# Kernel tuning notes

Measured on AMD Instinct MI355X. Metric: run time of the kernel, lower is better.

Reference implementation:

```python
import jax, jax.numpy as jnp
import numpy as np

D_MODEL = 1024
NUM_HEADS = 16
THETA = 10000.0
B, S = 4, 2048


def setup_inputs() -> dict:
    key = jax.random.key(0)
    ks = jax.random.split(key, 5)
    scale = 1.0 / np.sqrt(D_MODEL)  # keep logits in a sane range
    return {
        "q_proj_weight": jax.random.normal(ks[0], (D_MODEL, D_MODEL), jnp.float32) * scale,
        "k_proj_weight": jax.random.normal(ks[1], (D_MODEL, D_MODEL), jnp.float32) * scale,
        "v_proj_weight": jax.random.normal(ks[2], (D_MODEL, D_MODEL), jnp.float32) * scale,
        "o_proj_weight": jax.random.normal(ks[3], (D_MODEL, D_MODEL), jnp.float32) * scale,
        "in_features": jax.random.normal(ks[4], (B, S, D_MODEL), jnp.float32),
        "token_positions": jnp.arange(S, dtype=jnp.int32),
    }


def _rope(x, cos, sin):
    # interleaved-pair RoPE: pairs are (x[..., 2i], x[..., 2i+1])
    xe = x[..., 0::2]
    xo = x[..., 1::2]
    re = xe * cos - xo * sin
    ro = xe * sin + xo * cos
    return jnp.stack([re, ro], axis=-1).reshape(x.shape)


def reference(q_proj_weight, k_proj_weight, v_proj_weight, o_proj_weight,
              in_features, token_positions):
    Bv, Sv, _ = in_features.shape
    dk = D_MODEL // NUM_HEADS
    half = dk // 2

    q = in_features @ q_proj_weight.T
    k = in_features @ k_proj_weight.T
    v = in_features @ v_proj_weight.T
    # (B, S, D) -> (B, H, S, dk)
    q = q.reshape(Bv, Sv, NUM_HEADS, dk).transpose(0, 2, 1, 3)
    k = k.reshape(Bv, Sv, NUM_HEADS, dk).transpose(0, 2, 1, 3)
    v = v.reshape(Bv, Sv, NUM_HEADS, dk).transpose(0, 2, 1, 3)

    inv_freq = 1.0 / (THETA ** (jnp.arange(half, dtype=jnp.float32) / half))
    freqs = token_positions.astype(jnp.float32)[:, None] * inv_freq[None, :]  # (S, half)
    cos, sin = jnp.cos(freqs), jnp.sin(freqs)  # broadcast over (B, H, S, half)
    q = _rope(q, cos, sin)
    k = _rope(k, cos, sin)

    scores = jnp.einsum('bhqd,bhkd->bhqk', q, k) / np.sqrt(dk).astype(np.float32)
    causal = jnp.tril(jnp.ones((Sv, Sv), dtype=bool))
    scores = jnp.where(causal, scores, -jnp.inf)
    weights = jax.nn.softmax(scores, axis=-1)
    out = jnp.einsum('bhqk,bhkd->bhqd', weights, v)
    out = out.transpose(0, 2, 1, 3).reshape(Bv, Sv, D_MODEL)
    return out @ o_proj_weight.T
```

## Files before the change

### kernel.cpp

```cpp
#include <hip/hip_runtime.h>
#include <stdint.h>
#include <math.h>

#define NH 16
#define DK 64
#define S_LEN 2048
#define BB 4
#define DM 1024
#define M_TOT (BB*S_LEN)
#define KVT 64
#define KPAD 72
#define QB 128

#define BM 256
#define BN 128
#define BK 64
#define NTK (DM/BK)
#define LDS_A_BUF (BM*BK)
#define LDS_B_BUF (BN*BK)

typedef __attribute__((ext_vector_type(8))) short short8;
typedef __attribute__((ext_vector_type(4))) float floatx4;

typedef const __attribute__((address_space(1))) void gas_t;
typedef __attribute__((address_space(3))) void las_t;

__device__ __forceinline__ void glds16(const void* g, void* l){
  __builtin_amdgcn_global_load_lds((gas_t*)g, (las_t*)l, 16, 0, 0);
}

#define VMCNT3() asm volatile("s_waitcnt vmcnt(3)" ::: "memory")
#define VMCNT6() asm volatile("s_waitcnt vmcnt(6)" ::: "memory")
#define VMCNT0() asm volatile("s_waitcnt vmcnt(0)" ::: "memory")
#define LGKM0()  do{ asm volatile("s_waitcnt lgkmcnt(0)" ::: "memory"); __builtin_amdgcn_sched_barrier(0); }while(0)
#define BARRIER() asm volatile("s_barrier" ::: "memory")
#define SCHEDB() __builtin_amdgcn_sched_barrier(0)

__device__ __forceinline__ unsigned short f2bf(float f){
  unsigned int u = __float_as_uint(f);
  u += 0x7fffu + ((u >> 16) & 1u);
  return (unsigned short)(u >> 16);
}
__device__ __forceinline__ unsigned int pk_bf_trunc(float a, float b){
  return __builtin_amdgcn_perm(__float_as_uint(b), __float_as_uint(a), 0x07060302u);
}
__device__ __forceinline__ float fast_exp2(float x){
  return __builtin_amdgcn_exp2f(x);
}

__global__ void cast_kernel(const float* __restrict__ in, unsigned short* __restrict__ out, int n){
  int i = (blockIdx.x * blockDim.x + threadIdx.x) * 4;
  if (i < n){
    float4 v = *(const float4*)(in + i);
    ushort4 u;
    u.x = f2bf(v.x); u.y = f2bf(v.y); u.z = f2bf(v.z); u.w = f2bf(v.w);
    *(ushort4*)(out + i) = u;
  }
}
__global__ void cast4_kernel(const float* __restrict__ a, const float* __restrict__ b,
                             const float* __restrict__ c, const float* __restrict__ d,
                             unsigned short* __restrict__ oa, unsigned short* __restrict__ ob,
                             unsigned short* __restrict__ oc, unsigned short* __restrict__ od){
  int z = blockIdx.y;
  const float* s = (z==0)?a:(z==1)?b:(z==2)?c:d;
  unsigned short* o = (z==0)?oa:(z==1)?ob:(z==2)?oc:od;
  int i = (blockIdx.x * blockDim.x + threadIdx.x) * 4;
  float4 v = *(const float4*)(s + i);
  ushort4 u;
  u.x = f2bf(v.x); u.y = f2bf(v.y); u.z = f2bf(v.z); u.w = f2bf(v.w);
  *(ushort4*)(o + i) = u;
}

__device__ __forceinline__ void stage_part(const unsigned short* __restrict__ A,
                                           const unsigned short* __restrict__ Bm,
                                           int m0, int n0, int k0,
                                           unsigned short* As, unsigned short* Bs,
                                           int tid, int part)
{
  if (part == 0){
    #pragma unroll
    for (int j = 0; j < 2; j++){
      int c = j*512 + tid;
      int r = c >> 3;
      int sl = (c & 7) ^ (r & 7);
      glds16(&A[(size_t)(m0 + r)*DM + k0 + sl*8], (char*)As + (size_t)c*16);
    }
    int c = tid;
    int r = c >> 3;
    int sl = (c & 7) ^ (r & 7);
    glds16(&Bm[(size_t)(n0 + r)*DM + k0 + sl*8], (char*)Bs + (size_t)c*16);
  } else {
    #pragma unroll
    for (int j = 2; j < 4; j++){
      int c = j*512 + tid;
      int r = c >> 3;
      int sl = (c & 7) ^ (r & 7);
      glds16(&A[(size_t)(m0 + r)*DM + k0 + sl*8], (char*)As + (size_t)c*16);
    }
    int c = 512 + tid;
    int r = c >> 3;
    int sl = (c & 7) ^ (r & 7);
    glds16(&Bm[(size_t)(n0 + r)*DM + k0 + sl*8], (char*)Bs + (size_t)c*16);
  }
}

__device__ __forceinline__ void gemm_core(const unsigned short* __restrict__ A,
                                          const unsigned short* __restrict__ Bm,
                                          int m0, int n0, unsigned short* Ls,
                                          int tid, floatx4 (&acc)[4][4])
{
  unsigned short* AsB = Ls;
  unsigned short* BsB = Ls + 3*LDS_A_BUF;
  int wave = tid >> 6, lane = tid & 63;
  int l15 = lane & 15, quad = lane >> 4;
  int wm = (wave >> 1) * 64, wn = (wave & 1) * 64;
  int s0 = quad ^ (l15 & 7);

  short8 a01[2][2], a23[2][2], b[2][4][2];

  stage_part(A, Bm, m0, n0, 0,  AsB,             BsB,             tid, 0);
  stage_part(A, Bm, m0, n0, 0,  AsB,             BsB,             tid, 1);
  stage_part(A, Bm, m0, n0, BK, AsB + LDS_A_BUF, BsB + LDS_B_BUF, tid, 0);
  stage_part(A, Bm, m0, n0, BK, AsB + LDS_A_BUF, BsB + LDS_B_BUF, tid, 1);
  VMCNT6();
  BARRIER();
  #pragma unroll
  for (int mi = 0; mi < 2; mi++){
    const unsigned short* pr = AsB + (wm + mi*16 + l15)*BK;
    a01[mi][0] = *(const short8*)(pr + s0*8);
    a01[mi][1] = *(const short8*)(pr + (s0^4)*8);
  }
  #pragma unroll
  for (int ni = 0; ni < 4; ni++){
    const unsigned short* pr = BsB + (wn + ni*16 + l15)*BK;
    b[0][ni][0] = *(const short8*)(pr + s0*8);
    b[0][ni][1] = *(const short8*)(pr + (s0^4)*8);
  }

  #pragma unroll
  for (int t = 0; t < NTK; ++t){
    const int par = t & 1, nxt = par ^ 1;
    const unsigned short* Ab  = AsB + (t % 3)*LDS_A_BUF;
    const unsigned short* Abn = AsB + ((t+1) % 3)*LDS_A_BUF;
    const unsigned short* Bbn = BsB + ((t+1) % 3)*LDS_B_BUF;
    unsigned short* Ast = AsB + ((t+2) % 3)*LDS_A_BUF;
    unsigned short* Bst = BsB + ((t+2) % 3)*LDS_B_BUF;
    const int kst = (t + 2) * BK;

    LGKM0();
    #pragma unroll
    for (int mi = 0; mi < 2; mi++){
      const unsigned short* pr = Ab + (wm + (2+mi)*16 + l15)*BK;
      a23[mi][0] = *(const short8*)(pr + s0*8);
      a23[mi][1] = *(const short8*)(pr + (s0^4)*8);
    }
    if (t + 2 < NTK) stage_part(A, Bm, m0, n0, kst, Ast, Bst, tid, 0);
    SCHEDB();
    __builtin_amdgcn_s_setprio(1);
    #pragma unroll
    for (int mi = 0; mi < 2; mi++)
      #pragma unroll
      for (int ni = 0; ni < 4; ni++){
        acc[mi][ni] = __builtin_amdgcn_mfma_f32_16x16x32_bf16(a01[mi][0], b[par][ni][0], acc[mi][ni], 0, 0, 0);
        acc[mi][ni] = __builtin_amdgcn_mfma_f32_16x16x32_bf16(a01[mi][1], b[par][ni][1], acc[mi][ni], 0, 0, 0);
      }
    __builtin_amdgcn_s_setprio(0);
    if (t + 2 < NTK)      { VMCNT3(); }
    else if (t + 1 < NTK) { VMCNT0(); }
    BARRIER();

    LGKM0();
    if (t + 1 < NTK){
      #pragma unroll
      for (int mi = 0; mi < 2; mi++){
        const unsigned short* pr = Abn + (wm + mi*16 + l15)*BK;
        a01[mi][0] = *(const short8*)(pr + s0*8);
        a01[mi][1] = *(const short8*)(pr + (s0^4)*8);
      }
      #pragma unroll
      for (int ni = 0; ni < 4; ni++){
        const unsigned short* pr = Bbn + (wn + ni*16 + l15)*BK;
        b[nxt][ni][0] = *(const short8*)(pr + s0*8);
        b[nxt][ni][1] = *(const short8*)(pr + (s0^4)*8);
      }
    }
    if (t + 2 < NTK) stage_part(A, Bm, m0, n0, kst, Ast, Bst, tid, 1);
    SCHEDB();
    __builtin_amdgcn_s_setprio(1);
    #pragma unroll
    for (int mi = 0; mi < 2; mi++)
      #pragma unroll
      for (int ni = 0; ni < 4; ni++){
        acc[2+mi][ni] = __builtin_amdgcn_mfma_f32_16x16x32_bf16(a23[mi][0], b[par][ni][0], acc[2+mi][ni], 0, 0, 0);
        acc[2+mi][ni] = __builtin_amdgcn_mfma_f32_16x16x32_bf16(a23[mi][1], b[par][ni][1], acc[2+mi][ni], 0, 0, 0);
      }
    __builtin_amdgcn_s_setprio(0);
    if (t + 1 < NTK) BARRIER();
  }
}

__global__ __launch_bounds__(512, 2) void gemm_qkv(
    const unsigned short* __restrict__ Xb,
    const unsigned short* __restrict__ Wq,
    const unsigned short* __restrict__ Wk,
    const unsigned short* __restrict__ Wv,
    const int* __restrict__ pos,
    unsigned short* __restrict__ Qo,
    unsigned short* __restrict__ Ko,
    unsigned short* __restrict__ VTo)
{
  __shared__ __align__(16) unsigned short Ls[3*LDS_A_BUF + 3*LDS_B_BUF];
  int m0 = blockIdx.x * BM;
  int n0 = blockIdx.y * BN;
  int z  = blockIdx.z;
  const unsigned short* Bmat = (z == 0) ? Wq : ((z == 1) ? Wk : Wv);
  unsigned short* Out = (z == 0) ? Qo : ((z == 1) ? Ko : VTo);

  int tid = threadIdx.x;
  floatx4 acc[4][4] = {};
  gemm_core(Xb, Bmat, m0, n0, Ls, tid, acc);

  int wave = tid >> 6, lane = tid & 63;
  int l15 = lane & 15, quad = lane >> 4;
  int wm = (wave >> 1) * 64, wn = (wave & 1) * 64;

  if (z == 2){
    #pragma unroll
    for (int mi = 0; mi < 4; mi++){
      int row0 = m0 + wm + mi * 16 + quad * 4;
      int bb2 = row0 >> 11, sQ = row0 & (S_LEN - 1);
      #pragma unroll
      for (int ni = 0; ni < 4; ni++){
        int col = n0 + wn + ni * 16 + l15;
        int h = col >> 6, d = col & 63;
        ushort4 u;
        u.x = f2bf(acc[mi][ni][0]); u.y = f2bf(acc[mi][ni][1]);
        u.z = f2bf(acc[mi][ni][2]); u.w = f2bf(acc[mi][ni][3]);
        *(ushort4*)&Out[(((size_t)bb2 * NH + h) * DK + d) * S_LEN + sQ] = u;
      }
    }
  } else {
    const float SC = (z == 0) ? 0.180336879f : 1.0f;
    #pragma unroll
    for (int mi = 0; mi < 4; mi++){
      #pragma unroll
      for (int ni = 0; ni < 4; ni++){
        int col = n0 + wn + ni * 16 + l15;
        int h = col >> 6, d = col & 63;
        int fi = d >> 1, odd = d & 1;
        float invfrev = fast_exp2(-(float)fi * (13.2877123795494f / 32.0f)) * 0.15915494309f;
        #pragma unroll
        for (int r = 0; r < 4; r++){
          int row = m0 + wm + mi * 16 + quad * 4 + r;
          int bb2 = row >> 11, s = row & (S_LEN - 1);
          float p = (float)pos[s];
          float rev = p * invfrev;
          rev = rev - floorf(rev);
          float c  = __builtin_amdgcn_cosf(rev);
          float sn = __builtin_amdgcn_sinf(rev);
          float val = acc[mi][ni][r];
          float other = __shfl_xor(val, 1);
          float outv = odd ? (other * sn + val * c) : (val * c - other * sn);
          Out[(((size_t)bb2 * NH + h) * S_LEN + s) * DK + d] = f2bf(outv * SC);
        }
      }
    }
  }
}

__global__ __launch_bounds__(512, 2) void gemm_out(
    const unsigned short* __restrict__ Ab,
    const unsigned short* __restrict__ Wo,
    float* __restrict__ Out)
{
  __shared__ __align__(16) unsigned short Ls[3*LDS_A_BUF + 3*LDS_B_BUF];
  int m0 = blockIdx.x * BM;
  int n0 = blockIdx.y * BN;

  int tid = threadIdx.x;
  floatx4 acc[4][4] = {};
  gemm_core(Ab, Wo, m0, n0, Ls, tid, acc);

  int wave = tid >> 6, lane = tid & 63;
  int l15 = lane & 15, quad = lane >> 4;
  int wm = (wave >> 1) * 64, wn = (wave & 1) * 64;

  #pragma unroll
  for (int mi = 0; mi < 4; mi++){
    #pragma unroll
    for (int ni = 0; ni < 4; ni++){
      #pragma unroll
      for (int r = 0; r < 4; r++){
        int row = m0 + wm + mi * 16 + quad * 4 + r;
        int col = n0 + wn + ni * 16 + l15;
        Out[(size_t)row * DM + col] = acc[mi][ni][r];
      }
    }
  }
}

__global__ __launch_bounds__(256) void attn_kernel(
    const unsigned short* __restrict__ Qg,
    const unsigned short* __restrict__ Kg,
    const unsigned short* __restrict__ VTg,
    unsigned short* __restrict__ Ao)
{
  __shared__ __align__(16) unsigned short Ks[KVT * KPAD];
  __shared__ __align__(16) unsigned short Vs[DK * KPAD];
  __shared__ __align__(16) unsigned short Ps[4][32 * KPAD];

  int bh = blockIdx.x;
  int q0 = ((int)gridDim.y - 1 - (int)blockIdx.y) * QB;
  int tid = threadIdx.x, wave = tid >> 6, lane = tid & 63;
  int l15 = lane & 15, quad = lane >> 4;
  int qw = q0 + wave * 32;

  const unsigned short* Qb = Qg + (size_t)bh * S_LEN * DK;
  const unsigned short* Kb = Kg + (size_t)bh * S_LEN * DK;
  const unsigned short* Vb = VTg + (size_t)bh * DK * S_LEN;

  short8 aq[2][2];
  #pragma unroll
  for (int mi = 0; mi < 2; mi++){
    aq[mi][0] = *(const short8*)&Qb[(qw + mi * 16 + l15) * DK + quad * 8];
    aq[mi][1] = *(const short8*)&Qb[(qw + mi * 16 + l15) * DK + 32 + quad * 8];
  }

  floatx4 o[2][4] = {};
  float lsum[2][4] = {{0.f,0.f,0.f,0.f},{0.f,0.f,0.f,0.f}};

  int srow = tid >> 2;
  int scol = (tid & 3) * 16;
  int kpos = (srow & 3) * 16 + (srow >> 2);
  const unsigned short* Krow = Kb + (size_t)srow * DK + scol;
  const unsigned short* Vrow = Vb + (size_t)srow * S_LEN + scol;
  unsigned short* KsW = &Ks[kpos * KPAD + scol];
  unsigned short* VsW = &Vs[srow * KPAD + scol];

  int nt = q0 / KVT + 2;

  short8 kr0 = *(const short8*)(Krow);
  short8 kr1 = *(const short8*)(Krow + 8);
  short8 vr0 = *(const short8*)(Vrow);
  short8 vr1 = *(const short8*)(Vrow + 8);

  for (int kt = 0; kt < nt; kt++){
    int kv0 = kt * KVT;
    __syncthreads();
    *(short8*)(KsW)     = kr0;
    *(short8*)(KsW + 8) = kr1;
    *(short8*)(VsW)     = vr0;
    *(short8*)(VsW + 8) = vr1;
    if (kt + 1 < nt){
      int kvn = kv0 + KVT;
      kr0 = *(const short8*)(Krow + (size_t)kvn * DK);
      kr1 = *(const short8*)(Krow + (size_t)kvn * DK + 8);
      vr0 = *(const short8*)(Vrow + kvn);
      vr1 = *(const short8*)(Vrow + kvn + 8);
    }
    __syncthreads();

    if (kv0 <= qw + 31){
      floatx4 sc[2][4] = {};
      #pragma unroll
      for (int ni = 0; ni < 4; ni++){
        short8 bk0 = *(const short8*)&Ks[(ni * 16 + l15) * KPAD + quad * 8];
        short8 bk1 = *(const short8*)&Ks[(ni * 16 + l15) * KPAD + 32 + quad * 8];
        #pragma unroll
        for (int mi = 0; mi < 2; mi++){
          sc[mi][ni] = __builtin_amdgcn_mfma_f32_16x16x32_bf16(aq[mi][0], bk0, sc[mi][ni], 0, 0, 0);
          sc[mi][ni] = __builtin_amdgcn_mfma_f32_16x16x32_bf16(aq[mi][1], bk1, sc[mi][ni], 0, 0, 0);
        }
      }
      bool full = (kv0 + 63 <= qw);
      int kvb = kv0 + 4 * l15;
      #pragma unroll
      for (int mi = 0; mi < 2; mi++){
        #pragma unroll
        for (int r = 0; r < 4; r++){
          int qg = qw + mi * 16 + quad * 4 + r;
          float v0 = sc[mi][0][r], v1 = sc[mi][1][r], v2 = sc[mi][2][r], v3 = sc[mi][3][r];
          if (!full){
            v0 = (kvb     > qg) ? -INFINITY : v0;
            v1 = (kvb + 1 > qg) ? -INFINITY : v1;
            v2 = (kvb + 2 > qg) ? -INFINITY : v2;
            v3 = (kvb + 3 > qg) ? -INFINITY : v3;
          }
          float p0 = fast_exp2(v0);
          float p1 = fast_exp2(v1);
          float p2 = fast_exp2(v2);
          float p3 = fast_exp2(v3);
          lsum[mi][r] += (p0 + p1) + (p2 + p3);
          uint2 u;
          u.x = pk_bf_trunc(p0, p1);
          u.y = pk_bf_trunc(p2, p3);
          *(uint2*)&Ps[wave][(mi * 16 + quad * 4 + r) * KPAD + 4 * l15] = u;
        }
      }
      asm volatile("s_waitcnt lgkmcnt(0)" ::: "memory");
      short8 ap[2][2];
      #pragma unroll
      for (int mi = 0; mi < 2; mi++){
        ap[mi][0] = *(const short8*)&Ps[wave][(mi * 16 + l15) * KPAD + quad * 8];
        ap[mi][1] = *(const short8*)&Ps[wave][(mi * 16 + l15) * KPAD + 32 + quad * 8];
      }
      #pragma unroll
      for (int dt = 0; dt < 4; dt++){
        short8 bv0 = *(const short8*)&Vs[(dt * 16 + l15) * KPAD + quad * 8];
        short8 bv1 = *(const short8*)&Vs[(dt * 16 + l15) * KPAD + 32 + quad * 8];
        #pragma unroll
        for (int mi = 0; mi < 2; mi++){
          o[mi][dt] = __builtin_amdgcn_mfma_f32_16x16x32_bf16(ap[mi][0], bv0, o[mi][dt], 0, 0, 0);
          o[mi][dt] = __builtin_amdgcn_mfma_f32_16x16x32_bf16(ap[mi][1], bv1, o[mi][dt], 0, 0, 0);
        }
      }
    }
  }

  float linv[2][4];
  #pragma unroll
  for (int mi = 0; mi < 2; mi++){
    #pragma unroll
    for (int r = 0; r < 4; r++){
      float rs = lsum[mi][r];
      rs += __shfl_xor(rs, 1);
      rs += __shfl_xor(rs, 2);
      rs += __shfl_xor(rs, 4);
      rs += __shfl_xor(rs, 8);
      linv[mi][r] = 1.0f / rs;
    }
  }

  int bq = bh >> 4, hq = bh & 15;
  #pragma unroll
  for (int mi = 0; mi < 2; mi++){
    #pragma unroll
    for (int dt = 0; dt < 4; dt++){
      #pragma unroll
      for (int r = 0; r < 4; r++){
        float val = o[mi][dt][r] * linv[mi][r];
        int s = qw + mi * 16 + quad * 4 + r;
        int d = dt * 16 + l15;
        Ao[(((size_t)bq * S_LEN + s) * NH + hq) * DK + d] = f2bf(val);
      }
    }
  }
}

extern "C" void kernel_launch(void* const* d_in, const int* in_sizes, int n_in,
                              void* d_out, int out_size, void* d_ws, size_t ws_size,
                              hipStream_t stream) {
  (void)in_sizes; (void)n_in; (void)out_size; (void)ws_size;
  const float* Wq = (const float*)d_in[0];
  const float* Wk = (const float*)d_in[1];
  const float* Wv = (const float*)d_in[2];
  const float* Wo = (const float*)d_in[3];
  const float* X  = (const float*)d_in[4];
  const int* pos  = (const int*)d_in[5];
  float* out = (float*)d_out;

  char* ws = (char*)d_ws;
  const size_t MB = 1024 * 1024;
  unsigned short* Xb  = (unsigned short*)(ws);
  unsigned short* Wqb = (unsigned short*)(ws + 16 * MB);
  unsigned short* Wkb = (unsigned short*)(ws + 18 * MB);
  unsigned short* Wvb = (unsigned short*)(ws + 20 * MB);
  unsigned short* Wob = (unsigned short*)(ws + 22 * MB);
  unsigned short* Qb  = (unsigned short*)(ws + 24 * MB);
  unsigned short* Kb  = (unsigned short*)(ws + 40 * MB);
  unsigned short* Vb  = (unsigned short*)(ws + 56 * MB);
  unsigned short* Ab  = (unsigned short*)(ws + 72 * MB);

  cast_kernel<<<8192, 256, 0, stream>>>(X,  Xb,  M_TOT * DM);
  cast4_kernel<<<dim3(1024, 4), 256, 0, stream>>>(Wq, Wk, Wv, Wo, Wqb, Wkb, Wvb, Wob);

  gemm_qkv<<<dim3(M_TOT/BM, DM/BN, 3), 512, 0, stream>>>(Xb, Wqb, Wkb, Wvb, pos, Qb, Kb, Vb);
  attn_kernel<<<dim3(64, S_LEN / QB), 256, 0, stream>>>(Qb, Kb, Vb, Ab);
  gemm_out<<<dim3(M_TOT/BM, DM/BN), 512, 0, stream>>>(Ab, Wob, out);
}
```

Measured before the change: 239.8 us.

## Transpose attention MFMAs to keep P in registers and double-buffer K/V LDS

```diff
diff --git a/kernel.cpp b/kernel.cpp
--- a/kernel.cpp
+++ b/kernel.cpp
@@ -299,15 +299,14 @@
   }
 }
 
-__global__ __launch_bounds__(256) void attn_kernel(
+__global__ __launch_bounds__(256, 4) void attn_kernel(
     const unsigned short* __restrict__ Qg,
     const unsigned short* __restrict__ Kg,
     const unsigned short* __restrict__ VTg,
     unsigned short* __restrict__ Ao)
 {
-  __shared__ __align__(16) unsigned short Ks[KVT * KPAD];
-  __shared__ __align__(16) unsigned short Vs[DK * KPAD];
-  __shared__ __align__(16) unsigned short Ps[4][32 * KPAD];
+  __shared__ __align__(16) unsigned short Ks[2][KVT * KPAD];
+  __shared__ __align__(16) unsigned short Vs[2][DK * KPAD];
 
   int bh = blockIdx.x;
   int q0 = ((int)gridDim.y - 1 - (int)blockIdx.y) * QB;
@@ -326,18 +325,19 @@
     aq[mi][1] = *(const short8*)&Qb[(qw + mi * 16 + l15) * DK + 32 + quad * 8];
   }
 
-  floatx4 o[2][4] = {};
-  float lsum[2][4] = {{0.f,0.f,0.f,0.f},{0.f,0.f,0.f,0.f}};
+  floatx4 o2[2][4] = {};
+  float lsum[2] = {0.f, 0.f};
 
   int srow = tid >> 2;
   int scol = (tid & 3) * 16;
-  int kpos = (srow & 3) * 16 + (srow >> 2);
   const unsigned short* Krow = Kb + (size_t)srow * DK + scol;
   const unsigned short* Vrow = Vb + (size_t)srow * S_LEN + scol;
-  unsigned short* KsW = &Ks[kpos * KPAD + scol];
-  unsigned short* VsW = &Vs[srow * KPAD + scol];
 
   int nt = q0 / KVT + 2;
+
+  int sl0 = l15 + ((lane & 16) << 1);
+  int sl1 = sl0 + 16;
+  bool niHi = (lane & 32) != 0;
 
   short8 kr0 = *(const short8*)(Krow);
   short8 kr1 = *(const short8*)(Krow + 8);
@@ -346,11 +346,11 @@
 
   for (int kt = 0; kt < nt; kt++){
     int kv0 = kt * KVT;
-    __syncthreads();
-    *(short8*)(KsW)     = kr0;
-    *(short8*)(KsW + 8) = kr1;
-    *(short8*)(VsW)     = vr0;
-    *(short8*)(VsW + 8) = vr1;
+    int p = kt & 1;
+    *(short8*)&Ks[p][srow * KPAD + scol]     = kr0;
+    *(short8*)&Ks[p][srow * KPAD + scol + 8] = kr1;
+    *(short8*)&Vs[p][srow * KPAD + scol]     = vr0;
+    *(short8*)&Vs[p][srow * KPAD + scol + 8] = vr1;
     if (kt + 1 < nt){
       int kvn = kv0 + KVT;
       kr0 = *(const short8*)(Krow + (size_t)kvn * DK);
@@ -358,28 +358,32 @@
       vr0 = *(const short8*)(Vrow + kvn);
       vr1 = *(const short8*)(Vrow + kvn + 8);
     }
-    __syncthreads();
+    LGKM0();
+    BARRIER();
 
     if (kv0 <= qw + 31){
-      floatx4 sc[2][4] = {};
-      #pragma unroll
-      for (int ni = 0; ni < 4; ni++){
-        short8 bk0 = *(const short8*)&Ks[(ni * 16 + l15) * KPAD + quad * 8];
-        short8 bk1 = *(const short8*)&Ks[(ni * 16 + l15) * KPAD + 32 + quad * 8];
+      floatx4 s2[2][4] = {};
+      #pragma unroll
+      for (int ni = 0; ni < 4; ni++){
+        short8 bk0 = *(const short8*)&Ks[p][(ni * 16 + l15) * KPAD + quad * 8];
+        short8 bk1 = *(const short8*)&Ks[p][(ni * 16 + l15) * KPAD + 32 + quad * 8];
         #pragma unroll
         for (int mi = 0; mi < 2; mi++){
-          sc[mi][ni] = __builtin_amdgcn_mfma_f32_16x16x32_bf16(aq[mi][0], bk0, sc[mi][ni], 0, 0, 0);
-          sc[mi][ni] = __builtin_amdgcn_mfma_f32_16x16x32_bf16(aq[mi][1], bk1, sc[mi][ni], 0, 0, 0);
+          s2[mi][ni] = __builtin_amdgcn_mfma_f32_16x16x32_bf16(bk0, aq[mi][0], s2[mi][ni], 0, 0, 0);
+          s2[mi][ni] = __builtin_amdgcn_mfma_f32_16x16x32_bf16(bk1, aq[mi][1], s2[mi][ni], 0, 0, 0);
         }
       }
       bool full = (kv0 + 63 <= qw);
-      int kvb = kv0 + 4 * l15;
+      short8 pw[2][2];
       #pragma unroll
       for (int mi = 0; mi < 2; mi++){
+        int qg = qw + mi * 16 + l15;
+        unsigned int u[4][2];
+        float ls = 0.f;
         #pragma unroll
-        for (int r = 0; r < 4; r++){
-          int qg = qw + mi * 16 + quad * 4 + r;
-          float v0 = sc[mi][0][r], v1 = sc[mi][1][r], v2 = sc[mi][2][r], v3 = sc[mi][3][r];
+        for (int ni = 0; ni < 4; ni++){
+          int kvb = kv0 + ni * 16 + quad * 4;
+          float v0 = s2[mi][ni][0], v1 = s2[mi][ni][1], v2 = s2[mi][ni][2], v3 = s2[mi][ni][3];
           if (!full){
             v0 = (kvb     > qg) ? -INFINITY : v0;
             v1 = (kvb + 1 > qg) ? -INFINITY : v1;
@@ -390,59 +394,63 @@
           float p1 = fast_exp2(v1);
           float p2 = fast_exp2(v2);
           float p3 = fast_exp2(v3);
-          lsum[mi][r] += (p0 + p1) + (p2 + p3);
-          uint2 u;
-          u.x = pk_bf_trunc(p0, p1);
-          u.y = pk_bf_trunc(p2, p3);
-          *(uint2*)&Ps[wave][(mi * 16 + quad * 4 + r) * KPAD + 4 * l15] = u;
+          ls += (p0 + p1) + (p2 + p3);
+          u[ni][0] = pk_bf_trunc(p0, p1);
+          u[ni][1] = pk_bf_trunc(p2, p3);
         }
-      }
-      asm volatile("s_waitcnt lgkmcnt(0)" ::: "memory");
-      short8 ap[2][2];
-      #pragma unroll
-      for (int mi = 0; mi < 2; mi++){
-        ap[mi][0] = *(const short8*)&Ps[wave][(mi * 16 + l15) * KPAD + quad * 8];
-        ap[mi][1] = *(const short8*)&Ps[wave][(mi * 16 + l15) * KPAD + 32 + quad * 8];
+        lsum[mi] += ls;
+        #pragma unroll
+        for (int h2 = 0; h2 < 2; h2++){
+          unsigned int we0 = (unsigned int)__shfl((int)u[2*h2][0],   sl0);
+          unsigned int wo0 = (unsigned int)__shfl((int)u[2*h2+1][0], sl0);
+          unsigned int we1 = (unsigned int)__shfl((int)u[2*h2][1],   sl0);
+          unsigned int wo1 = (unsigned int)__shfl((int)u[2*h2+1][1], sl0);
+          unsigned int we2 = (unsigned int)__shfl((int)u[2*h2][0],   sl1);
+          unsigned int wo2 = (unsigned int)__shfl((int)u[2*h2+1][0], sl1);
+          unsigned int we3 = (unsigned int)__shfl((int)u[2*h2][1],   sl1);
+          unsigned int wo3 = (unsigned int)__shfl((int)u[2*h2+1][1], sl1);
+          union { unsigned int w[4]; short8 v; } pb;
+          pb.w[0] = niHi ? wo0 : we0;
+          pb.w[1] = niHi ? wo1 : we1;
+          pb.w[2] = niHi ? wo2 : we2;
+          pb.w[3] = niHi ? wo3 : we3;
+          pw[mi][h2] = pb.v;
+        }
       }
       #pragma unroll
       for (int dt = 0; dt < 4; dt++){
-        short8 bv0 = *(const short8*)&Vs[(dt * 16 + l15) * KPAD + quad * 8];
-        short8 bv1 = *(const short8*)&Vs[(dt * 16 + l15) * KPAD + 32 + quad * 8];
+        short8 bv0 = *(const short8*)&Vs[p][(dt * 16 + l15) * KPAD + quad * 8];
+        short8 bv1 = *(const short8*)&Vs[p][(dt * 16 + l15) * KPAD + 32 + quad * 8];
         #pragma unroll
         for (int mi = 0; mi < 2; mi++){
-          o[mi][dt] = __builtin_amdgcn_mfma_f32_16x16x32_bf16(ap[mi][0], bv0, o[mi][dt], 0, 0, 0);
-          o[mi][dt] = __builtin_amdgcn_mfma_f32_16x16x32_bf16(ap[mi][1], bv1, o[mi][dt], 0, 0, 0);
+          o2[mi][dt] = __builtin_amdgcn_mfma_f32_16x16x32_bf16(bv0, pw[mi][0], o2[mi][dt], 0, 0, 0);
+          o2[mi][dt] = __builtin_amdgcn_mfma_f32_16x16x32_bf16(bv1, pw[mi][1], o2[mi][dt], 0, 0, 0);
         }
       }
     }
   }
 
-  float linv[2][4];
+  float linv[2];
   #pragma unroll
   for (int mi = 0; mi < 2; mi++){
-    #pragma unroll
-    for (int r = 0; r < 4; r++){
-      float rs = lsum[mi][r];
-      rs += __shfl_xor(rs, 1);
-      rs += __shfl_xor(rs, 2);
-      rs += __shfl_xor(rs, 4);
-      rs += __shfl_xor(rs, 8);
-      linv[mi][r] = 1.0f / rs;
-    }
+    float rs = lsum[mi];
+    rs += __shfl_xor(rs, 16);
+    rs += __shfl_xor(rs, 32);
+    linv[mi] = 1.0f / rs;
   }
 
   int bq = bh >> 4, hq = bh & 15;
   #pragma unroll
   for (int mi = 0; mi < 2; mi++){
+    int s = qw + mi * 16 + l15;
     #pragma unroll
     for (int dt = 0; dt < 4; dt++){
-      #pragma unroll
-      for (int r = 0; r < 4; r++){
-        float val = o[mi][dt][r] * linv[mi][r];
-        int s = qw + mi * 16 + quad * 4 + r;
-        int d = dt * 16 + l15;
-        Ao[(((size_t)bq * S_LEN + s) * NH + hq) * DK + d] = f2bf(val);
-      }
+      ushort4 uo;
+      uo.x = f2bf(o2[mi][dt][0] * linv[mi]);
+      uo.y = f2bf(o2[mi][dt][1] * linv[mi]);
+      uo.z = f2bf(o2[mi][dt][2] * linv[mi]);
+      uo.w = f2bf(o2[mi][dt][3] * linv[mi]);
+      *(ushort4*)&Ao[(((size_t)bq * S_LEN + s) * NH + hq) * DK + dt * 16 + quad * 4] = uo;
     }
   }
 }
```

Result: slower. 270.5 us (+12.8%).
